# Optimization experiments

Hardware: AMD Instinct MI355X
Metric: run time of the kernel (lower is better)

## Reference

```python
import jax, jax.numpy as jnp
import numpy as np

B, S, D, K = 16, 1024, 512, 4
DIL = (1, 2, 4, 8)
EPS_BN = 1e-5
EPS_LN = 1e-5


def _edge_conv1d(x, w, b, dilation):
    # x: [B, C, S], w: [O, C, k]; replicate ('edge') padding keeps length S
    p = (w.shape[-1] - 1) * dilation // 2
    xp = jnp.pad(x, ((0, 0), (0, 0), (p, p)), mode='edge')
    y = jax.lax.conv_general_dilated(xp, w, (1,), 'VALID', rhs_dilation=(dilation,),
                                     dimension_numbers=('NCH', 'OIH', 'NCH'))
    return y + b[None, :, None]


def setup_inputs() -> dict:
    key = jax.random.key(0)
    ks = jax.random.split(key, 16)
    g = lambda i, shape, s: jax.random.normal(ks[i], shape, jnp.float32) * s
    return {
        'x': g(0, (B, S, D), 1.0),
        'conv_w': g(1, (4, D, D, 3), 0.02),
        'conv_b': jnp.zeros((4, D), jnp.float32),
        'fusion_w': g(2, (D, 4 * D), 0.02),
        'fusion_b': jnp.zeros((D,), jnp.float32),
        'refine_w': g(3, (D, D, 3), 0.02),
        'refine_b': jnp.zeros((D,), jnp.float32),
        'hyp1_w': g(4, (D, D, 3), 0.02),
        'hyp1_b': jnp.zeros((D,), jnp.float32),
        'bn_gamma': jnp.ones((D,), jnp.float32),
        'bn_beta': jnp.zeros((D,), jnp.float32),
        'hyp2_w': g(5, (D // 2, D, 3), 0.02),
        'hyp2_b': jnp.zeros((D // 2,), jnp.float32),
        'proj_w': g(6, (2 * K, D // 2), 0.05),
        'proj_b': jnp.zeros((2 * K,), jnp.float32),
        'gate_w': g(7, (D, D), 0.02),
        'gate_b': jnp.zeros((D,), jnp.float32),
        'base_w': g(8, (D, D), 0.02),
        'base_b': jnp.zeros((D,), jnp.float32),
        'wav_w': g(9, (K, D, D), 0.02),
        'wav_b': jnp.zeros((K, D), jnp.float32),
        'ln_gamma': jnp.ones((D,), jnp.float32),
        'ln_beta': jnp.zeros((D,), jnp.float32),
    }


def _forward(x, conv_w, conv_b, fusion_w, fusion_b, refine_w, refine_b,
             hyp1_w, hyp1_b, bn_gamma, bn_beta, hyp2_w, hyp2_b,
             proj_w, proj_b, gate_w, gate_b, base_w, base_b,
             wav_w, wav_b, ln_gamma, ln_beta):
    residual = x
    x_in = jnp.transpose(x, (0, 2, 1))                      # [B, D, S]
    # ---- FFT trend/seasonal split ----
    fx = jnp.fft.rfft(x_in, axis=2)
    cutoff = S // 10
    mask = (jnp.arange(fx.shape[2]) < cutoff).astype(fx.dtype)
    x_seasonal = jnp.fft.irfft(fx * mask, n=S, axis=2)       # [B, D, S]
    x_smooth = x_seasonal
    x_spike = x_in - x_seasonal
    # ---- iterative dilated-conv smoothing (dropout = identity, eval mode) ----
    for _ in range(2):  # iterations
        outs = [jax.nn.gelu(_edge_conv1d(x_smooth, conv_w[i], conv_b[i], DIL[i]),
                            approximate=False)
                for i in range(4)]
        x_concat = jnp.concatenate(outs, axis=1)             # [B, 4D, S]
        x_smooth = jnp.einsum('oc,bcs->bos', fusion_w, x_concat) + fusion_b[None, :, None]
        x_spike = _edge_conv1d(x_in - x_smooth, refine_w, refine_b, 1)
    x_smooth_t = jnp.transpose(x_smooth, (0, 2, 1))          # [B, S, D]
    x_spike_t = jnp.transpose(x_spike, (0, 2, 1))            # [B, S, D]
    # ---- hypernet (BatchNorm in eval mode: running mean 0, var 1) ----
    h = _edge_conv1d(x_smooth, hyp1_w, hyp1_b, 1)
    h = h / jnp.sqrt(1.0 + EPS_BN) * bn_gamma[None, :, None] + bn_beta[None, :, None]
    h = jax.nn.silu(h)
    h = jax.nn.silu(_edge_conv1d(h, hyp2_w, hyp2_b, 1))      # [B, D/2, S]
    cnn_feat = jnp.mean(h, axis=2)                           # AdaptiveAvgPool1d(1)
    params = (cnn_feat @ proj_w.T + proj_b).reshape(B, 1, K, 2)
    dyn_a = jax.nn.softplus(params[..., 0]) + 0.01           # [B, 1, K]
    dyn_b = jax.nn.sigmoid(params[..., 1]) * S               # [B, 1, K]
    # ---- wavelet-KAN base path: Linear(silu(x_smooth)) ----
    base_out = jnp.einsum('bsd,ed->bse', jax.nn.silu(x_smooth_t), base_w) + base_b
    # ---- wavelet path: mexican-hat wavelets over sequence positions ----
    pos = jnp.arange(S, dtype=x.dtype)[None, :, None]        # [1, S, 1]
    u = (pos - dyn_b) / dyn_a                                # [B, S, K]
    c = 2.0 / (np.sqrt(3.0) * np.pi ** 0.25)
    psi = c * (1.0 - u * u) * jnp.exp(-0.5 * u * u)          # [B, S, K]
    z = jnp.einsum('bsd,kde->bkse', x_spike_t, wav_w)        # per-wavelet linear
    kan_out = jnp.einsum('bsk,bkse->bse', psi, z) + jnp.einsum('bsk,ke->bse', psi, wav_b)
    amp = jax.nn.sigmoid(base_out @ gate_w.T + gate_b) * 2.0
    x_out = base_out + kan_out * amp
    # ---- residual + LayerNorm ----
    y = x_out + residual
    mu = jnp.mean(y, axis=-1, keepdims=True)
    var = jnp.var(y, axis=-1, keepdims=True)
    return (y - mu) / jnp.sqrt(var + EPS_LN) * ln_gamma + ln_beta


def reference(x, conv_w, conv_b, fusion_w, fusion_b, refine_w, refine_b,
              hyp1_w, hyp1_b, bn_gamma, bn_beta, hyp2_w, hyp2_b,
              proj_w, proj_b, gate_w, gate_b, base_w, base_b,
              wav_w, wav_b, ln_gamma, ln_beta):
    return _forward(x, conv_w, conv_b, fusion_w, fusion_b, refine_w, refine_b,
                    hyp1_w, hyp1_b, bn_gamma, bn_beta, hyp2_w, hyp2_b,
                    proj_w, proj_b, gate_w, gate_b, base_w, base_b,
                    wav_w, wav_b, ln_gamma, ln_beta)
```

## Files before the change

### kernel.cpp

```cpp
#include <hip/hip_runtime.h>
#include <hip/hip_bf16.h>
#include <math.h>

#define NB 16
#define SS 1024
#define DD 512
#define HD 256

typedef unsigned short US;
typedef short bf16x8 __attribute__((ext_vector_type(8)));
typedef float f32x4 __attribute__((ext_vector_type(4)));
typedef __attribute__((address_space(1))) const void gv1;
typedef __attribute__((address_space(3))) void lv3;

static __device__ __forceinline__ float b2sf(US u){ return __uint_as_float(((unsigned)u)<<16); }
static __device__ __forceinline__ US f2b(float f){
  __hip_bfloat16 h = __float2bfloat16(f);
  union { __hip_bfloat16 h; US u; } c; c.h = h; return c.u;
}
static __device__ __forceinline__ float rd(const void* __restrict__ p, long i, int isf){
  return isf ? ((const float*)p)[i] : b2sf(((const US*)p)[i]);
}

__global__ void k_detect(const void* __restrict__ x, int* __restrict__ flag){
  const US* u = (const US*)x;
  int t = threadIdx.x;
  float m = 0.f;
  for (int i = t; i < 4096; i += 256){
    float v = fabsf(b2sf(u[i]));
    if (isnan(v) || isinf(v)) v = 1e30f;
    m = fmaxf(m, v);
  }
  for (int off = 32; off; off >>= 1) m = fmaxf(m, __shfl_down(m, off));
  __shared__ float sh[4];
  if ((t & 63) == 0) sh[t >> 6] = m;
  __syncthreads();
  if (t == 0){
    float mm = fmaxf(fmaxf(sh[0], sh[1]), fmaxf(sh[2], sh[3]));
    flag[0] = (mm > 1e6f) ? 1 : 0;
  }
}

struct WTab { const void* src[8]; long start[9]; int type[8]; int C[8]; };
__global__ void k_prep_w(WTab wt, US* __restrict__ dst, const int* __restrict__ fl){
  int isf = fl[0];
  long i = (long)blockIdx.x*256 + threadIdx.x;
  if (i >= wt.start[8]) return;
  int s = 0;
  while (i >= wt.start[s+1]) s++;
  long r = i - wt.start[s];
  long si;
  if (wt.type[s] == 0){
    int C = wt.C[s]; long oc3 = 3L*C;
    int o = (int)(r / oc3); int rr = (int)(r - (long)o*oc3); int t = rr / C; int c = rr - t*C;
    si = ((long)o*C + c)*3 + t;
  } else if (wt.type[s] == 1){
    int k = (int)(r >> 18); int e = (int)((r >> 9) & 511); int d = (int)(r & 511);
    si = ((long)(k*512 + d))*512 + e;
  } else si = r;
  dst[i] = f2b(rd(wt.src[s], si, isf));
}

struct FTab { const void* src[14]; int start[15]; };
__global__ void k_cvt_all(FTab ft, float* __restrict__ dst, const int* __restrict__ fl){
  int isf = fl[0];
  int i = blockIdx.x*256 + threadIdx.x;
  if (i >= ft.start[14]) return;
  int s = 0;
  while (i >= ft.start[s+1]) s++;
  dst[i] = rd(ft.src[s], i - ft.start[s], isf);
}

__global__ void k_build_g(float* __restrict__ g){
  int d = blockIdx.x*256 + threadIdx.x;
  if (d >= SS) return;
  float s = 1.f;
  for (int k = 1; k < 102; ++k){
    int r = (k*d) & (SS-1);
    s += 2.f * cosf(6.28318530718f * (float)r * (1.f/SS));
  }
  g[d] = s * (1.f/SS);
}
__global__ void k_build_cmat(const float* __restrict__ g, US* __restrict__ cm){
  int i = blockIdx.x*256 + threadIdx.x;
  if (i >= SS*SS) return;
  int t = i >> 10, s = i & (SS-1);
  cm[i] = f2b(g[(s - t) & (SS-1)]);
}
__global__ __launch_bounds__(256) void k_transpose_b(const void* __restrict__ x, US* __restrict__ xt, const int* __restrict__ fl){
  int isf = fl[0];
  __shared__ float tl[32][33];
  int b = blockIdx.z, s0 = blockIdx.x*32, d0 = blockIdx.y*32;
  int tx = threadIdx.x & 31, ty = threadIdx.x >> 5;
  for (int i = ty; i < 32; i += 8)
    tl[i][tx] = rd(x, ((long)(b*SS + s0+i))*DD + d0+tx, isf);
  __syncthreads();
  for (int i = ty; i < 32; i += 8)
    xt[((long)(b*DD + d0+i))*SS + s0+tx] = f2b(tl[tx][i]);
}

template<int EPI, bool TAPPED>
__global__ __launch_bounds__(512, 4) void k_dbuf(
    const US* __restrict__ A, const US* __restrict__ Bact, void* __restrict__ Out,
    int NYB, int K, long sBbytes, int ldbB, int dil,
    long sOut, int ldo, const float* __restrict__ bias)
{
  __shared__ US ring[36864];
  const int bx = blockIdx.x;
  const int ny = bx % NYB, b = bx / NYB;
  const int m0 = blockIdx.y*256, n0 = ny*128;
  const int dd = (TAPPED && dil < 0) ? (1 << (m0 >> 9)) : dil;
  const char* Bb = (const char*)Bact + (long)b*sBbytes;
  const int tid = threadIdx.x;
  const int lane = tid & 63, w = tid >> 6;
  const int wm = w >> 1, wn = w & 1;
  const int col = lane & 15, g = lane >> 4;
  const int NTs = K >> 5;

  int offA[4], offB[4];
  #pragma unroll
  for (int mf = 0; mf < 4; mf++){
    int r = wm*64 + mf*16 + col;
    int wg = ((r & 1) << 2) | g;
    offA[mf] = (r >> 1)*128 + ((wg ^ ((r >> 1) & 7)) << 4);
  }
  #pragma unroll
  for (int nf = 0; nf < 4; nf++){
    int r = wn*64 + nf*16 + col;
    int wg = ((r & 1) << 2) | g;
    offB[nf] = (r >> 1)*128 + ((wg ^ ((r >> 1) & 7)) << 4);
  }
  int rlA[2], ggA[2];
  #pragma unroll
  for (int j = 0; j < 2; j++){
    int c = w*128 + j*64 + lane;
    int R = c >> 3, f = c & 7;
    int wg = f ^ (R & 7);
    rlA[j] = 2*R + (wg >> 2);
    ggA[j] = wg & 3;
  }
  int rlB, ggB;
  {
    int R = tid >> 3, f = tid & 7;
    int wg = f ^ (R & 7);
    rlB = 2*R + (wg >> 2);
    ggB = wg & 3;
  }

  auto slotOf = [](int t){ int s = t % 3; return s; };

  auto stageA = [&](int t){
    int slot = t % 3, kb = t << 5;
    #pragma unroll
    for (int j = 0; j < 2; j++){
      const char* ga = (const char*)A + ((long)(m0 + rlA[j])*K + kb + ggA[j]*8)*2;
      __builtin_amdgcn_global_load_lds((gv1*)ga, (lv3*)&ring[slot*8192 + w*1024 + j*512], 16, 0, 0);
    }
  };
  auto stageB = [&](int t){
    int slot = t % 3, kb = t << 5;
    int c0 = TAPPED ? (kb & 511) : kb;
    int tapoff = TAPPED ? (((kb >> 9) - 1)*dd) : 0;
    int brow = n0 + rlB + tapoff;
    if (TAPPED) brow = brow < 0 ? 0 : (brow > SS-1 ? SS-1 : brow);
    const char* gb = Bb + (long)brow*ldbB + (c0 + ggB*8)*2;
    __builtin_amdgcn_global_load_lds((gv1*)gb, (lv3*)&ring[24576 + slot*4096 + w*512], 16, 0, 0);
  };

  f32x4 acc[4][4];
  #pragma unroll
  for (int i = 0; i < 4; i++)
    #pragma unroll
    for (int j = 0; j < 4; j++) acc[i][j] = (f32x4){0.f,0.f,0.f,0.f};

  stageA(0); stageB(0);
  stageA(1); stageB(1);
  stageA(2); stageB(2);
  asm volatile("s_waitcnt vmcnt(6)" ::: "memory");
  __builtin_amdgcn_s_barrier();

  for (int ks = 0; ks < NTs; ++ks){
    int slot = ks % 3;
    const char* As = (const char*)&ring[slot*8192];
    const char* Bs = (const char*)&ring[24576 + slot*4096];
    bf16x8 af[4], bf[4];
    #pragma unroll
    for (int mf = 0; mf < 4; mf++) af[mf] = *(const bf16x8*)(As + offA[mf]);
    #pragma unroll
    for (int nf = 0; nf < 4; nf++) bf[nf] = *(const bf16x8*)(Bs + offB[nf]);
    asm volatile("s_waitcnt lgkmcnt(0)" ::: "memory");
    __builtin_amdgcn_s_barrier();
    if (ks + 3 < NTs){ stageA(ks + 3); stageB(ks + 3); }
    __builtin_amdgcn_s_setprio(1);
    #pragma unroll
    for (int mf = 0; mf < 4; mf++)
      #pragma unroll
      for (int nf = 0; nf < 4; nf++)
        acc[mf][nf] = __builtin_amdgcn_mfma_f32_16x16x32_bf16(af[mf], bf[nf], acc[mf][nf], 0, 0, 0);
    __builtin_amdgcn_s_setprio(0);
    if (ks < NTs - 3)       asm volatile("s_waitcnt vmcnt(6)" ::: "memory");
    else if (ks == NTs - 3) asm volatile("s_waitcnt vmcnt(3)" ::: "memory");
    else if (ks == NTs - 2) asm volatile("s_waitcnt vmcnt(0)" ::: "memory");
    __builtin_amdgcn_s_barrier();
  }
  (void)slotOf;

  US* tile = ring;
  #pragma unroll
  for (int mf = 0; mf < 4; mf++){
    int m_l = wm*64 + mf*16 + g*4;
    float4 bb = *(const float4*)&bias[m0 + m_l];
    const float* bp = (const float*)&bb;
    #pragma unroll
    for (int nf = 0; nf < 4; nf++){
      int n_l = wn*64 + nf*16 + col;
      f32x4 v = acc[mf][nf];
      US pk[4];
      #pragma unroll
      for (int r = 0; r < 4; r++){
        float val = v[r] + bp[r];
        if (EPI == 1) val = 0.5f*val*(1.f + erff(val*0.70710678f));
        pk[r] = f2b(val);
      }
      long byte = (long)n_l*512 + ((((m_l >> 3) ^ (n_l & 7)) << 4) | ((m_l & 7)*2));
      *(int2*)((char*)tile + byte) = *(int2*)pk;
    }
  }
  __syncthreads();
  #pragma unroll
  for (int p = 0; p < 8; p++){
    int chunk = p*512 + tid;
    int rr = chunk >> 5, cg = chunk & 31;
    int4 vv = *(const int4*)((const char*)tile + (long)rr*512 + ((cg ^ (rr & 7)) << 4));
    *(int4*)((US*)Out + (long)b*sOut + (long)(n0 + rr)*ldo + m0 + cg*8) = vv;
  }
}

template<int EPI, bool TAPPED>
__global__ __launch_bounds__(256) void k_mfma(
    const US* __restrict__ A, const US* __restrict__ Bact, void* __restrict__ Out,
    int NYB, int K, long sBbytes, int ldbB, int dil,
    long sOut, int ldo,
    const float* __restrict__ bias, const float* __restrict__ s1v, const float* __restrict__ s2v,
    const float* __restrict__ psiP, const void* __restrict__ xres,
    US* __restrict__ aux1, US* __restrict__ aux2, const int* __restrict__ fl)
{
  __shared__ alignas(16) US shb[2*128*64];
  __shared__ float psh[(EPI==4) ? 512 : 4];
  US* As = shb;
  US* Bs = shb + 128*64;
  const int bx = blockIdx.x;
  const int ny = bx % NYB;
  const int b  = bx / NYB;
  const int m00 = blockIdx.y*128, n0 = ny*128;
  const int dd = (TAPPED && dil < 0) ? (1 << (m00 >> 9)) : dil;
  const char* Bb = (const char*)Bact + (long)b*sBbytes;
  const int tid = threadIdx.x;
  const int lane = tid & 63, w = tid >> 6;
  const int wr = w >> 1, wc = w & 1;
  const int col = lane & 15, g = lane >> 4;

  if (EPI == 4){
    for (int i = tid; i < 512; i += 256)
      psh[i] = psiP[(long)b*4096 + (i >> 7)*SS + n0 + (i & 127)];
  }

  f32x4 acc[4][4];
  f32x4 facc[4][4];
  if (EPI == 4){
    #pragma unroll
    for (int i = 0; i < 4; i++)
      #pragma unroll
      for (int j = 0; j < 4; j++) facc[i][j] = (f32x4){0.f,0.f,0.f,0.f};
  }

  int rows_[4], sls_[4];
  #pragma unroll
  for (int i = 0; i < 4; i++){
    int c = w*256 + i*64 + lane;
    rows_[i] = c >> 3;
    sls_[i] = (c & 7) ^ ((c >> 3) & 7);
  }

  const int NKC = (EPI == 4) ? 4 : 1;
  for (int kc = 0; kc < NKC; ++kc){
    #pragma unroll
    for (int i = 0; i < 4; i++)
      #pragma unroll
      for (int j = 0; j < 4; j++) acc[i][j] = (f32x4){0.f,0.f,0.f,0.f};

    for (int k0 = 0; k0 < K; k0 += 64){
      const int c0 = TAPPED ? (k0 & 511) : k0;
      const int tapoff = TAPPED ? (((k0 >> 9) - 1)*dd) : 0;
      __syncthreads();
      #pragma unroll
      for (int i = 0; i < 4; i++){
        const long arow = (long)(m00 + rows_[i]) + (EPI==4 ? kc*512 : 0);
        const char* ga = (const char*)A + (arow*K + k0)*2 + sls_[i]*16;
        __builtin_amdgcn_global_load_lds((gv1*)ga, (lv3*)&As[(w*256 + i*64)*8], 16, 0, 0);
        int brow = n0 + rows_[i] + tapoff;
        if (TAPPED) brow = brow < 0 ? 0 : (brow > SS-1 ? SS-1 : brow);
        const char* gb = Bb + (long)brow*ldbB + c0*2 + sls_[i]*16;
        __builtin_amdgcn_global_load_lds((gv1*)gb, (lv3*)&Bs[(w*256 + i*64)*8], 16, 0, 0);
      }
      __syncthreads();
      #pragma unroll
      for (int kk = 0; kk < 2; kk++){
        bf16x8 af[4], bf[4];
        #pragma unroll
        for (int f = 0; f < 4; f++){
          int rowa = wr*64 + f*16 + col;
          int sla = (g + kk*4) ^ (rowa & 7);
          af[f] = *(const bf16x8*)&As[rowa*64 + sla*8];
          int rowb = wc*64 + f*16 + col;
          int slb = (g + kk*4) ^ (rowb & 7);
          bf[f] = *(const bf16x8*)&Bs[rowb*64 + slb*8];
        }
        #pragma unroll
        for (int fm = 0; fm < 4; fm++)
          #pragma unroll
          for (int fn = 0; fn < 4; fn++)
            acc[fm][fn] = __builtin_amdgcn_mfma_f32_16x16x32_bf16(af[fm], bf[fn], acc[fm][fn], 0, 0, 0);
      }
    }

    if (EPI == 4){
      #pragma unroll
      for (int fm = 0; fm < 4; fm++){
        const int mm_l = wr*64 + fm*16 + g*4;
        float bb[4];
        #pragma unroll
        for (int r = 0; r < 4; r++) bb[r] = bias[kc*512 + m00 + mm_l + r];
        #pragma unroll
        for (int fn = 0; fn < 4; fn++){
          float p = psh[kc*128 + wc*64 + fn*16 + col];
          #pragma unroll
          for (int r = 0; r < 4; r++)
            facc[fm][fn][r] += p * (acc[fm][fn][r] + bb[r]);
        }
      }
    }
  }

  __syncthreads();
  US* tile = shb;
  #pragma unroll
  for (int fm = 0; fm < 4; fm++){
    const int mm_l = wr*64 + fm*16 + g*4;
    float bb[4];
    if (EPI == 0 || EPI == 2 || EPI == 3 || EPI == 6){
      #pragma unroll
      for (int r = 0; r < 4; r++) bb[r] = bias[m00 + mm_l + r];
    }
    #pragma unroll
    for (int fn = 0; fn < 4; fn++){
      const int nn_l = wc*64 + fn*16 + col;
      f32x4 v = (EPI == 4) ? facc[fm][fn] : acc[fm][fn];
      if (EPI == 5){
        #pragma unroll
        for (int r = 0; r < 4; r++){
          int row = mm_l + r;
          int byte = row*256 + ((nn_l*2) ^ ((row & 7) << 4));
          *(US*)((char*)tile + byte) = f2b(v[r]);
        }
      } else {
        US pk[4];
        #pragma unroll
        for (int r = 0; r < 4; r++){
          float val = v[r];
          if (EPI != 4) val += bb[r];
          if (EPI == 2){ int m = m00 + mm_l + r; val = val*(s1v[m]*0.99999500f) + s2v[m]; val = val/(1.f + expf(-val)); }
          if (EPI == 3){ val = val/(1.f + expf(-val)); }
          pk[r] = f2b(val);
        }
        int byte = nn_l*256 + ((mm_l*2) ^ ((nn_l & 7) << 4));
        *(int2*)((char*)tile + byte) = *(int2*)pk;
      }
    }
  }
  __syncthreads();
  const int r0 = tid >> 4, c = tid & 15;
  const int isf = (EPI == 6) ? fl[0] : 0;
  #pragma unroll
  for (int p = 0; p < 8; p++){
    int r = p*16 + r0;
    int4 vv = *(const int4*)((const char*)tile + r*256 + ((c*16) ^ ((r & 7) << 4)));
    long obase = (EPI == 5) ? ((long)b*sOut + (long)(m00 + r)*ldo + n0)
                            : ((long)b*sOut + (long)(n0 + r)*ldo + m00);
    *(int4*)((US*)Out + obase + c*8) = vv;
    if (EPI == 6){
      long eb = obase + c*8;
      const US* vp = (const US*)&vv;
      US dpk[8], lpk[8];
      #pragma unroll
      for (int q = 0; q < 8; q++){
        float sv = b2sf(vp[q]);
        float xv = rd(xres, eb + q, isf);
        dpk[q] = f2b(xv - sv);
        lpk[q] = f2b(sv/(1.f + expf(-sv)));
      }
      *(int4*)&aux1[eb] = *(int4*)dpk;
      *(int4*)&aux2[eb] = *(int4*)lpk;
    }
  }
}

__global__ __launch_bounds__(256) void k_pool1(const US* __restrict__ h2, float* __restrict__ part){
  int blk = blockIdx.x;
  int b = blk >> 3, ch = blk & 7;
  int c = threadIdx.x;
  float s = 0.f;
  for (int t = ch*128; t < ch*128 + 128; t++) s += b2sf(h2[((long)(b*SS + t))*HD + c]);
  part[(blk << 8) | c] = s;
}
__global__ __launch_bounds__(256) void k_pool2(const float* __restrict__ part, float* __restrict__ feat){
  int b = blockIdx.x, c = threadIdx.x;
  float s = 0.f;
  for (int ch = 0; ch < 8; ch++) s += part[((b*8 + ch) << 8) | c];
  feat[b*HD + c] = s * (1.f/SS);
}
__global__ void k_params(const float* __restrict__ feat, const float* __restrict__ pw,
                         const float* __restrict__ pb, float* __restrict__ dynA, float* __restrict__ dynB){
  int t = threadIdx.x;
  if (t >= 128) return;
  int b = t >> 3, j = t & 7;
  float s = pb[j];
  for (int c = 0; c < HD; c++) s += feat[b*HD + c]*pw[j*HD + c];
  int k = j >> 1;
  if ((j & 1) == 0){
    float sp = s > 20.f ? s : log1pf(expf(s));
    dynA[b*4 + k] = sp + 0.01f;
  } else {
    dynB[b*4 + k] = 1024.f/(1.f + expf(-s));
  }
}
__global__ void k_psi(const float* __restrict__ dynA, const float* __restrict__ dynB, float* __restrict__ psi){
  int i = blockIdx.x*256 + threadIdx.x;
  if (i >= NB*4*SS) return;
  int b = i >> 12, k = (i >> 10) & 3, s = i & (SS-1);
  float u = ((float)s - dynB[b*4 + k]) / dynA[b*4 + k];
  psi[i] = 0.86732507f*(1.f - u*u)*expf(-0.5f*u*u);
}
__global__ __launch_bounds__(128) void k_final(const US* __restrict__ base, const US* __restrict__ kan,
    const US* __restrict__ gate, const void* __restrict__ x,
    void* __restrict__ out, const float* __restrict__ lng, const float* __restrict__ lnb,
    const int* __restrict__ fl){
  int isf = fl[0];
  long row = blockIdx.x;
  int t = threadIdx.x;
  long off = row*DD + t*4;
  ushort4 bs = *(const ushort4*)&base[off];
  ushort4 gt = *(const ushort4*)&gate[off];
  ushort4 kn = *(const ushort4*)&kan[off];
  float xv[4];
  if (isf){ float4 q = *(const float4*)((const float*)x + off); xv[0]=q.x; xv[1]=q.y; xv[2]=q.z; xv[3]=q.w; }
  else { ushort4 q = *(const ushort4*)((const US*)x + off); xv[0]=b2sf(q.x); xv[1]=b2sf(q.y); xv[2]=b2sf(q.z); xv[3]=b2sf(q.w); }
  float bv[4] = {b2sf(bs.x), b2sf(bs.y), b2sf(bs.z), b2sf(bs.w)};
  float gv[4] = {b2sf(gt.x), b2sf(gt.y), b2sf(gt.z), b2sf(gt.w)};
  const US* kp = (const US*)&kn;
  float y[4];
  float sm = 0.f, ssq = 0.f;
  #pragma unroll
  for (int r = 0; r < 4; r++){
    float amp = 2.f/(1.f + expf(-gv[r]));
    y[r] = bv[r] + b2sf(kp[r])*amp + xv[r];
    sm += y[r]; ssq += y[r]*y[r];
  }
  for (int o = 32; o; o >>= 1){ sm += __shfl_down(sm, o); ssq += __shfl_down(ssq, o); }
  __shared__ float sh[4];
  int lane = t & 63, wid = t >> 6;
  if (lane == 0){ sh[wid*2] = sm; sh[wid*2+1] = ssq; }
  __syncthreads();
  float S1 = sh[0] + sh[2], S2 = sh[1] + sh[3];
  float mean = S1*(1.f/DD), var = S2*(1.f/DD) - mean*mean;
  float rstd = rsqrtf(var + 1e-5f);
  #pragma unroll
  for (int r = 0; r < 4; r++){
    int d = t*4 + r;
    float val = (y[r] - mean)*rstd*lng[d] + lnb[d];
    if (isf) ((float*)out)[off + r] = val;
    else     ((US*)out)[off + r] = f2b(val);
  }
}

extern "C" void kernel_launch(void* const* d_in, const int* in_sizes, int n_in,
                              void* d_out, int out_size, void* d_ws, size_t ws_size,
                              hipStream_t stream){
  const void* x       = d_in[0];
  const void* conv_w  = d_in[1];
  const void* conv_b  = d_in[2];
  const void* fusion_w= d_in[3];
  const void* fusion_b= d_in[4];
  const void* refine_w= d_in[5];
  const void* refine_b= d_in[6];
  const void* hyp1_w  = d_in[7];
  const void* hyp1_b  = d_in[8];
  const void* bn_g    = d_in[9];
  const void* bn_b    = d_in[10];
  const void* hyp2_w  = d_in[11];
  const void* hyp2_b  = d_in[12];
  const void* proj_w  = d_in[13];
  const void* proj_b  = d_in[14];
  const void* gate_w  = d_in[15];
  const void* gate_b  = d_in[16];
  const void* base_w  = d_in[17];
  const void* base_b  = d_in[18];
  const void* wav_w   = d_in[19];
  const void* wav_b   = d_in[20];
  const void* ln_g    = d_in[21];
  const void* ln_b    = d_in[22];

  char* wsb = (char*)d_ws;
  long off = 0;
  auto AA = [&](long bytes)->char*{ char* p = wsb + off; off += (bytes + 255) & ~255L; return p; };
  US* smA   = (US*)AA((long)NB*SS*DD*2);
  US* smB   = (US*)AA((long)NB*SS*DD*2);
  US* xTh   = (US*)AA((long)NB*SS*DD*2);
  US* cc    = (US*)AA((long)NB*SS*2048*2);
  US* baseB = (US*)AA((long)NB*SS*DD*2);
  US* WBLK  = (US*)AA(7733248L*2);
  US* Cm    = (US*)AA(1024L*1024*2);
  float* gvec = (float*)AA(1024*4);
  float* FBLK = (float*)AA(11016L*4);
  float* feat = (float*)AA(16*256*4);
  float* part = (float*)AA(16*8*256*4);
  float* dynA = (float*)AA(64*4);
  float* dynB = (float*)AA(64*4);
  float* psi  = (float*)AA((long)NB*4*SS*4);
  int* flag   = (int*)AA(64);
  if ((size_t)off > ws_size) return;

  US* Wc  = WBLK;
  US* Wr  = Wc  + 3145728L;
  US* Wh1 = Wr  + 786432L;
  US* Wh2 = Wh1 + 786432L;
  US* Wwv = Wh2 + 393216L;
  US* Fw  = Wwv + 1048576L;
  US* BW  = Fw  + 1048576L;
  US* GW  = BW  + 262144L;
  float* cb_f = FBLK;
  float* fz_b = cb_f + 2048;
  float* rf_b = fz_b + 512;
  float* h1_b = rf_b + 512;
  float* h2_b = h1_b + 512;
  float* bs_b = h2_b + 256;
  float* gt_b = bs_b + 512;
  float* wv_b = gt_b + 512;
  float* bngf = wv_b + 2048;
  float* bnbf = bngf + 512;
  float* pwf  = bnbf + 512;
  float* pbf  = pwf  + 2048;
  float* lngf = pbf  + 8;
  float* lnbf = lngf + 512;
  US* spike = cc;
  US* baseO = cc + 8388608L;
  US* kanb  = cc + 16777216L;
  US* h2b   = cc + 25165824L;

  auto g1 = [](long n){ return dim3((unsigned)((n + 255)/256)); };
  const long sAct = (long)SS*DD*2;
  const long sCC  = (long)SS*2048*2;
  const long oAct = (long)SS*DD;
  const long oCC  = (long)SS*2048;
  const long oH2  = (long)SS*HD;

  k_detect<<<1, 256, 0, stream>>>(x, flag);

  { WTab wt;
    const void* srcs[8] = {conv_w, refine_w, hyp1_w, hyp2_w, wav_w, fusion_w, base_w, gate_w};
    long sizes[8] = {3145728, 786432, 786432, 393216, 1048576, 1048576, 262144, 262144};
    int types[8] = {0,0,0,0,1,2,2,2};
    int Cs[8]    = {512,512,512,512,0,0,0,0};
    long acc_ = 0;
    for (int i = 0; i < 8; i++){ wt.src[i]=srcs[i]; wt.start[i]=acc_; wt.type[i]=types[i]; wt.C[i]=Cs[i]; acc_ += sizes[i]; }
    wt.start[8] = acc_;
    k_prep_w<<<g1(acc_), 256, 0, stream>>>(wt, WBLK, flag);
  }
  { FTab ft;
    const void* srcs[14] = {conv_b, fusion_b, refine_b, hyp1_b, hyp2_b, base_b, gate_b,
                            wav_b, bn_g, bn_b, proj_w, proj_b, ln_g, ln_b};
    int sizes[14] = {2048,512,512,512,256,512,512,2048,512,512,2048,8,512,512};
    int acc_ = 0;
    for (int i = 0; i < 14; i++){ ft.src[i]=srcs[i]; ft.start[i]=acc_; acc_ += sizes[i]; }
    ft.start[14] = acc_;
    k_cvt_all<<<g1(acc_), 256, 0, stream>>>(ft, FBLK, flag);
  }
  k_build_g<<<g1(SS), 256, 0, stream>>>(gvec);
  k_build_cmat<<<g1((long)SS*SS), 256, 0, stream>>>(gvec, Cm);
  k_transpose_b<<<dim3(SS/32, DD/32, NB), 256, 0, stream>>>(x, xTh, flag);

  k_mfma<5,false><<<dim3(4*NB, 8), 256, 0, stream>>>(Cm, xTh, smA,
      4, 1024, (long)DD*SS*2, SS*2, 0, oAct, DD,
      nullptr, nullptr, nullptr, nullptr, nullptr, nullptr, nullptr, nullptr);

  k_dbuf<1,true><<<dim3(8*NB, 8), 512, 0, stream>>>(Wc, smA, cc,
      8, 1536, sAct, DD*2, -1, oCC, 2048, cb_f);
  k_mfma<0,false><<<dim3(8*NB, 4), 256, 0, stream>>>(Fw, cc, smB,
      8, 2048, sCC, 4096, 0, oAct, DD,
      fz_b, nullptr, nullptr, nullptr, nullptr, nullptr, nullptr, nullptr);
  k_dbuf<1,true><<<dim3(8*NB, 8), 512, 0, stream>>>(Wc, smB, cc,
      8, 1536, sAct, DD*2, -1, oCC, 2048, cb_f);
  k_mfma<6,false><<<dim3(8*NB, 4), 256, 0, stream>>>(Fw, cc, smA,
      8, 2048, sCC, 4096, 0, oAct, DD,
      fz_b, nullptr, nullptr, nullptr, x, smB, baseB, flag);

  k_mfma<0,true><<<dim3(8*NB, 4), 256, 0, stream>>>(Wr, smB, spike,
      8, 1536, sAct, DD*2, 1, oAct, DD,
      rf_b, nullptr, nullptr, nullptr, nullptr, nullptr, nullptr, nullptr);

  k_mfma<2,true><<<dim3(8*NB, 4), 256, 0, stream>>>(Wh1, smA, xTh,
      8, 1536, sAct, DD*2, 1, oAct, DD,
      h1_b, bngf, bnbf, nullptr, nullptr, nullptr, nullptr, nullptr);
  k_mfma<3,true><<<dim3(8*NB, 2), 256, 0, stream>>>(Wh2, xTh, h2b,
      8, 1536, sAct, DD*2, 1, oH2, HD,
      h2_b, nullptr, nullptr, nullptr, nullptr, nullptr, nullptr, nullptr);
  k_pool1<<<NB*8, 256, 0, stream>>>(h2b, part);
  k_pool2<<<NB, 256, 0, stream>>>(part, feat);
  k_params<<<1, 128, 0, stream>>>(feat, pwf, pbf, dynA, dynB);
  k_psi<<<g1(NB*4*SS), 256, 0, stream>>>(dynA, dynB, psi);

  k_mfma<0,false><<<dim3(8*NB, 4), 256, 0, stream>>>(BW, baseB, baseO,
      8, 512, sAct, DD*2, 0, oAct, DD,
      bs_b, nullptr, nullptr, nullptr, nullptr, nullptr, nullptr, nullptr);
  k_mfma<0,false><<<dim3(8*NB, 4), 256, 0, stream>>>(GW, baseO, xTh,
      8, 512, sAct, DD*2, 0, oAct, DD,
      gt_b, nullptr, nullptr, nullptr, nullptr, nullptr, nullptr, nullptr);

  k_mfma<4,false><<<dim3(8*NB, 4), 256, 0, stream>>>(Wwv, spike, kanb,
      8, 512, sAct, DD*2, 0, oAct, DD,
      wv_b, nullptr, nullptr, psi, nullptr, nullptr, nullptr, nullptr);

  k_final<<<NB*SS, 128, 0, stream>>>(baseO, kanb, xTh, x, d_out, lngf, lnbf, flag);
}
```

Before: 665.9 us.

## Shrink tapped conv GEMM tile to 128x128 and double-buffer LDS fragment reads

The multi-dilation conv GEMM now uses a 128x128 tile with 256 threads instead of 256x128 with 512, which doubles the grid in M and shrinks the LDS ring. The main loop is unrolled by two with register double-buffering: the next step's LDS fragments are loaded while the current step's MFMAs run, which drops the barrier that used to sit between the LDS read and the compute. The aim is to hide LDS latency and raise occupancy. The cost is less reuse per block, since each B tile is now loaded by twice as many blocks.

```diff
diff --git a/kernel.cpp b/kernel.cpp
--- a/kernel.cpp
+++ b/kernel.cpp
@@ -100,15 +100,15 @@
 }
 
 template<int EPI, bool TAPPED>
-__global__ __launch_bounds__(512, 4) void k_dbuf(
+__global__ __launch_bounds__(256, 3) void k_pipe(
     const US* __restrict__ A, const US* __restrict__ Bact, void* __restrict__ Out,
     int NYB, int K, long sBbytes, int ldbB, int dil,
     long sOut, int ldo, const float* __restrict__ bias)
 {
-  __shared__ US ring[36864];
+  __shared__ alignas(16) US ring[24576];
   const int bx = blockIdx.x;
   const int ny = bx % NYB, b = bx / NYB;
-  const int m0 = blockIdx.y*256, n0 = ny*128;
+  const int m0 = blockIdx.y*128, n0 = ny*128;
   const int dd = (TAPPED && dil < 0) ? (1 << (m0 >> 9)) : dil;
   const char* Bb = (const char*)Bact + (long)b*sBbytes;
   const int tid = threadIdx.x;
@@ -130,41 +130,35 @@
     int wg = ((r & 1) << 2) | g;
     offB[nf] = (r >> 1)*128 + ((wg ^ ((r >> 1) & 7)) << 4);
   }
-  int rlA[2], ggA[2];
+  int rl[2], gg[2];
   #pragma unroll
   for (int j = 0; j < 2; j++){
     int c = w*128 + j*64 + lane;
     int R = c >> 3, f = c & 7;
     int wg = f ^ (R & 7);
-    rlA[j] = 2*R + (wg >> 2);
-    ggA[j] = wg & 3;
-  }
-  int rlB, ggB;
-  {
-    int R = tid >> 3, f = tid & 7;
-    int wg = f ^ (R & 7);
-    rlB = 2*R + (wg >> 2);
-    ggB = wg & 3;
-  }
-
-  auto slotOf = [](int t){ int s = t % 3; return s; };
+    rl[j] = 2*R + (wg >> 2);
+    gg[j] = wg & 3;
+  }
 
   auto stageA = [&](int t){
     int slot = t % 3, kb = t << 5;
     #pragma unroll
     for (int j = 0; j < 2; j++){
-      const char* ga = (const char*)A + ((long)(m0 + rlA[j])*K + kb + ggA[j]*8)*2;
-      __builtin_amdgcn_global_load_lds((gv1*)ga, (lv3*)&ring[slot*8192 + w*1024 + j*512], 16, 0, 0);
+      const char* ga = (const char*)A + ((long)(m0 + rl[j])*K + kb + gg[j]*8)*2;
+      __builtin_amdgcn_global_load_lds((gv1*)ga, (lv3*)&ring[slot*4096 + w*1024 + j*512], 16, 0, 0);
     }
   };
   auto stageB = [&](int t){
     int slot = t % 3, kb = t << 5;
     int c0 = TAPPED ? (kb & 511) : kb;
     int tapoff = TAPPED ? (((kb >> 9) - 1)*dd) : 0;
-    int brow = n0 + rlB + tapoff;
-    if (TAPPED) brow = brow < 0 ? 0 : (brow > SS-1 ? SS-1 : brow);
-    const char* gb = Bb + (long)brow*ldbB + (c0 + ggB*8)*2;
-    __builtin_amdgcn_global_load_lds((gv1*)gb, (lv3*)&ring[24576 + slot*4096 + w*512], 16, 0, 0);
+    #pragma unroll
+    for (int j = 0; j < 2; j++){
+      int brow = n0 + rl[j] + tapoff;
+      if (TAPPED) brow = brow < 0 ? 0 : (brow > SS-1 ? SS-1 : brow);
+      const char* gb = Bb + (long)brow*ldbB + (c0 + gg[j]*8)*2;
+      __builtin_amdgcn_global_load_lds((gv1*)gb, (lv3*)&ring[12288 + slot*4096 + w*1024 + j*512], 16, 0, 0);
+    }
   };
 
   f32x4 acc[4][4];
@@ -176,34 +170,54 @@
   stageA(0); stageB(0);
   stageA(1); stageB(1);
   stageA(2); stageB(2);
-  asm volatile("s_waitcnt vmcnt(6)" ::: "memory");
+  asm volatile("s_waitcnt vmcnt(4)" ::: "memory");
   __builtin_amdgcn_s_barrier();
 
-  for (int ks = 0; ks < NTs; ++ks){
-    int slot = ks % 3;
-    const char* As = (const char*)&ring[slot*8192];
-    const char* Bs = (const char*)&ring[24576 + slot*4096];
-    bf16x8 af[4], bf[4];
-    #pragma unroll
-    for (int mf = 0; mf < 4; mf++) af[mf] = *(const bf16x8*)(As + offA[mf]);
-    #pragma unroll
-    for (int nf = 0; nf < 4; nf++) bf[nf] = *(const bf16x8*)(Bs + offB[nf]);
+  bf16x8 a0[4], b0[4], a1[4], b1[4];
+  {
+    const char* As_ = (const char*)&ring[0];
+    const char* Bs_ = (const char*)&ring[12288];
+    #pragma unroll
+    for (int f = 0; f < 4; f++){ a0[f] = *(const bf16x8*)(As_ + offA[f]); b0[f] = *(const bf16x8*)(Bs_ + offB[f]); }
     asm volatile("s_waitcnt lgkmcnt(0)" ::: "memory");
-    __builtin_amdgcn_s_barrier();
-    if (ks + 3 < NTs){ stageA(ks + 3); stageB(ks + 3); }
-    __builtin_amdgcn_s_setprio(1);
-    #pragma unroll
-    for (int mf = 0; mf < 4; mf++)
-      #pragma unroll
-      for (int nf = 0; nf < 4; nf++)
-        acc[mf][nf] = __builtin_amdgcn_mfma_f32_16x16x32_bf16(af[mf], bf[nf], acc[mf][nf], 0, 0, 0);
-    __builtin_amdgcn_s_setprio(0);
-    if (ks < NTs - 3)       asm volatile("s_waitcnt vmcnt(6)" ::: "memory");
-    else if (ks == NTs - 3) asm volatile("s_waitcnt vmcnt(3)" ::: "memory");
-    else if (ks == NTs - 2) asm volatile("s_waitcnt vmcnt(0)" ::: "memory");
-    __builtin_amdgcn_s_barrier();
-  }
-  (void)slotOf;
+    __builtin_amdgcn_sched_barrier(0);
+  }
+
+#define PIPE_BODY(cA, cB, nA, nB, t)                                             \
+  {                                                                              \
+    if ((t) + 1 < NTs){                                                          \
+      int sl = ((t) + 1) % 3;                                                    \
+      const char* As_ = (const char*)&ring[sl*4096];                             \
+      const char* Bs_ = (const char*)&ring[12288 + sl*4096];                     \
+      nA[0] = *(const bf16x8*)(As_ + offA[0]);                                   \
+      nA[1] = *(const bf16x8*)(As_ + offA[1]);                                   \
+      nA[2] = *(const bf16x8*)(As_ + offA[2]);                                   \
+      nA[3] = *(const bf16x8*)(As_ + offA[3]);                                   \
+      nB[0] = *(const bf16x8*)(Bs_ + offB[0]);                                   \
+      nB[1] = *(const bf16x8*)(Bs_ + offB[1]);                                   \
+      nB[2] = *(const bf16x8*)(Bs_ + offB[2]);                                   \
+      nB[3] = *(const bf16x8*)(Bs_ + offB[3]);                                   \
+    }                                                                            \
+    if ((t) + 3 < NTs){ stageA((t) + 3); stageB((t) + 3); }                      \
+    __builtin_amdgcn_s_setprio(1);                                               \
+    _Pragma("unroll")                                                            \
+    for (int mf = 0; mf < 4; mf++)                                               \
+      _Pragma("unroll")                                                          \
+      for (int nf = 0; nf < 4; nf++)                                             \
+        acc[mf][nf] = __builtin_amdgcn_mfma_f32_16x16x32_bf16(cA[mf], cB[nf], acc[mf][nf], 0, 0, 0); \
+    __builtin_amdgcn_s_setprio(0);                                               \
+    asm volatile("s_waitcnt lgkmcnt(0)" ::: "memory");                           \
+    __builtin_amdgcn_sched_barrier(0);                                           \
+    if ((t) < NTs - 3) asm volatile("s_waitcnt vmcnt(4)" ::: "memory");          \
+    else               asm volatile("s_waitcnt vmcnt(0)" ::: "memory");          \
+    __builtin_amdgcn_s_barrier();                                                \
+  }
+
+  for (int ks = 0; ks < NTs; ks += 2){
+    PIPE_BODY(a0, b0, a1, b1, ks);
+    PIPE_BODY(a1, b1, a0, b0, ks + 1);
+  }
+#undef PIPE_BODY
 
   US* tile = ring;
   #pragma unroll
@@ -222,17 +236,17 @@
         if (EPI == 1) val = 0.5f*val*(1.f + erff(val*0.70710678f));
         pk[r] = f2b(val);
       }
-      long byte = (long)n_l*512 + ((((m_l >> 3) ^ (n_l & 7)) << 4) | ((m_l & 7)*2));
+      int byte = n_l*256 + ((m_l*2) ^ ((n_l & 7) << 4));
       *(int2*)((char*)tile + byte) = *(int2*)pk;
     }
   }
   __syncthreads();
+  const int r0 = tid >> 4, c = tid & 15;
   #pragma unroll
   for (int p = 0; p < 8; p++){
-    int chunk = p*512 + tid;
-    int rr = chunk >> 5, cg = chunk & 31;
-    int4 vv = *(const int4*)((const char*)tile + (long)rr*512 + ((cg ^ (rr & 7)) << 4));
-    *(int4*)((US*)Out + (long)b*sOut + (long)(n0 + rr)*ldo + m0 + cg*8) = vv;
+    int r = p*16 + r0;
+    int4 vv = *(const int4*)((const char*)tile + r*256 + ((c*16) ^ ((r & 7) << 4)));
+    *(int4*)((US*)Out + (long)b*sOut + (long)(n0 + r)*ldo + m0 + c*8) = vv;
   }
 }
 
@@ -593,12 +607,12 @@
       4, 1024, (long)DD*SS*2, SS*2, 0, oAct, DD,
       nullptr, nullptr, nullptr, nullptr, nullptr, nullptr, nullptr, nullptr);
 
-  k_dbuf<1,true><<<dim3(8*NB, 8), 512, 0, stream>>>(Wc, smA, cc,
+  k_pipe<1,true><<<dim3(8*NB, 16), 256, 0, stream>>>(Wc, smA, cc,
       8, 1536, sAct, DD*2, -1, oCC, 2048, cb_f);
   k_mfma<0,false><<<dim3(8*NB, 4), 256, 0, stream>>>(Fw, cc, smB,
       8, 2048, sCC, 4096, 0, oAct, DD,
       fz_b, nullptr, nullptr, nullptr, nullptr, nullptr, nullptr, nullptr);
-  k_dbuf<1,true><<<dim3(8*NB, 8), 512, 0, stream>>>(Wc, smB, cc,
+  k_pipe<1,true><<<dim3(8*NB, 16), 256, 0, stream>>>(Wc, smB, cc,
       8, 1536, sAct, DD*2, -1, oCC, 2048, cb_f);
   k_mfma<6,false><<<dim3(8*NB, 4), 256, 0, stream>>>(Fw, cc, smA,
       8, 2048, sCC, 4096, 0, oAct, DD,
```

Result: slower. 694.4 us (+4.3%).
